# Optimization experiments

Measured on AMD Instinct MI355X. Metric: run time of the kernel, lower is better.

The kernel has to match this reference:

```python
import jax, jax.numpy as jnp
import numpy as np

B, S, D = 2, 2048, 1024
H, KD, VD = 16, 64, 64


def setup_inputs() -> dict:
    key = jax.random.key(0)
    ks = jax.random.split(key, 12)
    s = 1.0 / np.sqrt(D)
    return {
        "q": jax.random.normal(ks[0], (B, S, D), jnp.float32),
        "k": jax.random.normal(ks[1], (B, S, D), jnp.float32),
        "v": jax.random.normal(ks[2], (B, S, D), jnp.float32),
        "mask": jnp.ones((S, S), jnp.int32),
        "Wq": jax.random.normal(ks[3], (D, H * KD), jnp.float32) * s,
        "bq": jnp.zeros((H * KD,), jnp.float32),
        "Wk": jax.random.normal(ks[4], (D, H * KD), jnp.float32) * s,
        "bk": jnp.zeros((H * KD,), jnp.float32),
        "Wv": jax.random.normal(ks[5], (D, H * VD), jnp.float32) * s,
        "bv": jnp.zeros((H * VD,), jnp.float32),
        "Wo": jax.random.normal(ks[6], (H * VD, D), jnp.float32) * (1.0 / np.sqrt(H * VD)),
        "bo": jnp.zeros((D,), jnp.float32),
    }


def reference(q, k, v, mask, Wq, bq, Wk, bk, Wv, bv, Wo, bo):
    bs = q.shape[0]
    # projections -> [B, H, S, d]
    qh = (q @ Wq + bq).reshape(bs, -1, H, KD).transpose(0, 2, 1, 3)
    kh = (k @ Wk + bk).reshape(bs, -1, H, KD).transpose(0, 2, 1, 3)
    vh = (v @ Wv + bv).reshape(bs, -1, H, VD).transpose(0, 2, 1, 3)
    scores = jnp.einsum("bhqd,bhkd->bhqk", qh, kh) / np.sqrt(KD)
    scores = jnp.where(mask[None, None, :, :] == 0, -1e9, scores)
    probs = jax.nn.softmax(scores, axis=-1)  # dropout is identity in eval
    attn = jnp.einsum("bhqk,bhkd->bhqd", probs, vh)
    concat = attn.transpose(0, 2, 1, 3).reshape(bs, -1, H * VD)
    return concat @ Wo + bo
```

## Files before the change

### kernel.cpp

```cpp
#include <hip/hip_runtime.h>
#include <stdint.h>

typedef __attribute__((ext_vector_type(8))) short short8;
typedef __attribute__((ext_vector_type(4))) float f32x4;
typedef __attribute__((ext_vector_type(16))) float f32x16;
typedef __attribute__((ext_vector_type(2))) unsigned int u32x2;

constexpr int Bc = 2, Sc = 2048, Dc = 1024, Hc = 16;
constexpr int MR = Bc * Sc;
#define CSC 0.18033688011112042f

static __device__ __forceinline__ unsigned short f2bf(float f) {
    union { float f; uint32_t u; } v; v.f = f;
    uint32_t u = v.u;
    u += 0x7FFFu + ((u >> 16) & 1u);
    return (unsigned short)(u >> 16);
}

static __device__ __forceinline__ uint32_t cvtpk(float lo, float hi) {
    uint32_t r;
    asm("v_cvt_pk_bf16_f32 %0, %1, %2" : "=v"(r) : "v"(lo), "v"(hi));
    return r;
}

static __device__ __forceinline__ float exp2a(float x) {
    float r;
    asm("v_exp_f32 %0, %1" : "=v"(r) : "v"(x));
    return r;
}

static __device__ __forceinline__ void gload_lds16(const void* g, void* l) {
    __builtin_amdgcn_global_load_lds(
        (const __attribute__((address_space(1))) unsigned int*)g,
        (__attribute__((address_space(3))) unsigned int*)l, 16, 0, 0);
}

__global__ void transpose_w_kernel(const float* __restrict__ Wq, const float* __restrict__ Wk,
                                   const float* __restrict__ Wv, const float* __restrict__ Wo,
                                   unsigned short* __restrict__ out) {
    __shared__ unsigned short tile[64][65];
    const float* W = (blockIdx.z == 0) ? Wq : (blockIdx.z == 1) ? Wk
                   : (blockIdx.z == 2) ? Wv : Wo;
    unsigned short* Wt = out + (size_t)blockIdx.z * (size_t)Dc * Dc;
    int n0 = blockIdx.x * 64, k0 = blockIdx.y * 64;
    int c = threadIdx.x & 63, r0 = threadIdx.x >> 6;
#pragma unroll
    for (int rr = 0; rr < 16; rr++) {
        int r = r0 + rr * 4;
        tile[r][c] = f2bf(W[(size_t)(k0 + r) * Dc + n0 + c]);
    }
    __syncthreads();
#pragma unroll
    for (int rr = 0; rr < 16; rr++) {
        int r = r0 + rr * 4;
        Wt[(size_t)(n0 + r) * Dc + k0 + c] = tile[c][r];
    }
}

__global__ __launch_bounds__(256, 2)
void gemm_qkv_kernel(const float* __restrict__ Xq, const float* __restrict__ Xk,
                     const float* __restrict__ Xv,
                     const unsigned short* __restrict__ Wt,
                     const float* __restrict__ bq, const float* __restrict__ bk,
                     const float* __restrict__ bv,
                     unsigned short* __restrict__ Qp,
                     unsigned short* __restrict__ Kp,
                     unsigned short* __restrict__ Vt)
{
    __shared__ unsigned short POOL[24576];
    unsigned short* Alds = POOL;
    unsigned short* Bl0  = POOL + 8192;
    unsigned short* Bl1  = POOL + 16384;
    const int lane = threadIdx.x & 63;
    const int wave = threadIdx.x >> 6;
    const int g = lane >> 4, r = lane & 15;
    const int r7 = r & 7;
    const int wr = wave >> 1, wc = wave & 1;
    const int tM = blockIdx.x * 128, tN = blockIdx.y * 128;
    const int m_blk = tN >> 10;
    const float* Af = (m_blk == 0) ? Xq : (m_blk == 1) ? Xk : Xv;
    const float* bias = (m_blk == 0) ? bq : (m_blk == 1) ? bk : bv;

    f32x4 acc[4][4] = {};

    const int lrow = lane >> 3, lun = lane & 7;
    const int lswz = (lun ^ lrow) * 8;
    const float* asrc[4];
    const unsigned short* bsrc[4];
#pragma unroll
    for (int i = 0; i < 4; i++) {
        int c = wave * 4 + i;
        int row = c * 8 + lrow;
        asrc[i] = Af + (size_t)(tM + row) * 1024 + lun * 8;
        bsrc[i] = Wt + (size_t)(tN + row) * 1024 + lswz;
    }

#pragma unroll
    for (int i = 0; i < 4; i++)
        gload_lds16(bsrc[i], (void*)(Bl0 + (wave * 4 + i) * 512));
    __builtin_amdgcn_sched_barrier(0);
    float4 afA[4][2];
#pragma unroll
    for (int i = 0; i < 4; i++) {
        afA[i][0] = *(const float4*)(asrc[i]);
        afA[i][1] = *(const float4*)(asrc[i] + 4);
    }

    unsigned short* Bcur = Bl0;
    unsigned short* Bnxt = Bl1;

    int sw[2];
    sw[0] = ((0 * 4 + g) ^ r7) * 8;
    sw[1] = ((1 * 4 + g) ^ r7) * 8;

    for (int kt = 0; kt < 1024; kt += 64) {
        if (kt < 960) {
#pragma unroll
            for (int i = 0; i < 4; i++)
                gload_lds16(bsrc[i] + kt + 64, (void*)(Bnxt + (wave * 4 + i) * 512));
        }
        __builtin_amdgcn_sched_barrier(0);

#pragma unroll
        for (int i = 0; i < 4; i++) {
            int c = wave * 4 + i;
            union { uint32_t u[4]; short8 s; } pk;
            pk.u[0] = cvtpk(afA[i][0].x, afA[i][0].y);
            pk.u[1] = cvtpk(afA[i][0].z, afA[i][0].w);
            pk.u[2] = cvtpk(afA[i][1].x, afA[i][1].y);
            pk.u[3] = cvtpk(afA[i][1].z, afA[i][1].w);
            *(short8*)(Alds + c * 512 + lrow * 64 + lswz) = pk.s;
        }
        if (kt < 960) {
#pragma unroll
            for (int i = 0; i < 4; i++) {
                afA[i][0] = *(const float4*)(asrc[i] + kt + 64);
                afA[i][1] = *(const float4*)(asrc[i] + kt + 68);
            }
        }
        __builtin_amdgcn_sched_barrier(0);
        asm volatile("s_waitcnt lgkmcnt(0)" ::: "memory");
        __builtin_amdgcn_s_barrier();
        __builtin_amdgcn_sched_barrier(0);

#pragma unroll
        for (int ks = 0; ks < 2; ks++) {
            short8 av[4], bvv[4];
#pragma unroll
            for (int mf = 0; mf < 4; mf++)
                av[mf] = *(const short8*)(Alds + (wr * 64 + mf * 16 + r) * 64 + sw[ks]);
#pragma unroll
            for (int nf = 0; nf < 4; nf++)
                bvv[nf] = *(const short8*)(Bcur + (wc * 64 + nf * 16 + r) * 64 + sw[ks]);
#pragma unroll
            for (int mf = 0; mf < 4; mf++)
#pragma unroll
                for (int nf = 0; nf < 4; nf++)
                    acc[mf][nf] = __builtin_amdgcn_mfma_f32_16x16x32_bf16(av[mf], bvv[nf], acc[mf][nf], 0, 0, 0);
        }
        __builtin_amdgcn_sched_barrier(0);
        asm volatile("s_waitcnt lgkmcnt(0)" ::: "memory");
        __builtin_amdgcn_s_barrier();
        __builtin_amdgcn_sched_barrier(0);

        unsigned short* tb = Bcur; Bcur = Bnxt; Bnxt = tb;
    }

    const int cbase = (tN & 1023) + wc * 64;
    const int h = cbase >> 6;
    const int bblk = tM >> 11;
    const int tMs = tM & 2047;
    unsigned short* Ow = POOL + wave * 2304;
    const float scl = (m_blk == 0) ? CSC : 1.0f;

    if (m_blk < 2) {
        unsigned short* dstQ = (m_blk == 0) ? Qp : Kp;
#pragma unroll
        for (int p = 0; p < 2; p++) {
#pragma unroll
            for (int mf2 = 0; mf2 < 2; mf2++)
#pragma unroll
                for (int nf = 0; nf < 4; nf++)
#pragma unroll
                    for (int i = 0; i < 4; i++) {
                        float val = (acc[2 * p + mf2][nf][i] + bias[cbase + nf * 16 + r]) * scl;
                        Ow[(mf2 * 16 + g * 4 + i) * 72 + nf * 16 + r] = f2bf(val);
                    }
            asm volatile("s_waitcnt lgkmcnt(0)" ::: "memory");
#pragma unroll
            for (int r4 = 0; r4 < 4; r4++) {
                int sl = r4 * 8 + (lane >> 3), dc = (lane & 7) * 8;
                short8 vv = *(const short8*)(Ow + sl * 72 + dc);
                int s = tMs + wr * 64 + p * 32 + sl;
                *(short8*)(dstQ + (((size_t)(bblk * Hc + h)) * Sc + s) * 64 + dc) = vv;
            }
            asm volatile("s_waitcnt lgkmcnt(0)" ::: "memory");
        }
    } else {
#pragma unroll
        for (int p = 0; p < 2; p++) {
#pragma unroll
            for (int nf2 = 0; nf2 < 2; nf2++)
#pragma unroll
                for (int mf = 0; mf < 4; mf++)
#pragma unroll
                    for (int i = 0; i < 4; i++) {
                        float val = acc[mf][2 * p + nf2][i] + bias[cbase + (2 * p + nf2) * 16 + r];
                        Ow[(nf2 * 16 + r) * 72 + mf * 16 + g * 4 + i] = f2bf(val);
                    }
            asm volatile("s_waitcnt lgkmcnt(0)" ::: "memory");
#pragma unroll
            for (int r4 = 0; r4 < 4; r4++) {
                int dl = r4 * 8 + (lane >> 3), sc_ = (lane & 7) * 8;
                short8 vv = *(const short8*)(Ow + dl * 72 + sc_);
                int dk = p * 32 + dl;
                *(short8*)(Vt + ((size_t)(bblk * Hc + h) * 64 + dk) * Sc
                              + (tMs + wr * 64 + sc_)) = vv;
            }
            asm volatile("s_waitcnt lgkmcnt(0)" ::: "memory");
        }
    }
}

__global__ __launch_bounds__(256, 2)
void gemm_out_kernel(const unsigned short* __restrict__ A,
                     const unsigned short* __restrict__ Bt,
                     const float* __restrict__ bias,
                     float* __restrict__ Cout)
{
    __shared__ unsigned short Alds[128 * 64];
    __shared__ unsigned short Blds[128 * 64];
    const int lane = threadIdx.x & 63;
    const int wave = threadIdx.x >> 6;
    const int g = lane >> 4, r = lane & 15;
    const int wr = wave >> 1, wc = wave & 1;
    const int tM = blockIdx.x * 128, tN = blockIdx.y * 128;

    f32x4 acc[4][4] = {};

    for (int kt = 0; kt < 1024; kt += 64) {
        __syncthreads();
#pragma unroll
        for (int i = 0; i < 4; i++) {
            int c = wave * 4 + i;
            int row = c * 8 + (lane >> 3);
            int kcol = kt + (lane & 7) * 8;
            gload_lds16(A  + (size_t)(tM + row) * 1024 + kcol, (void*)(Alds + c * 512));
            gload_lds16(Bt + (size_t)(tN + row) * 1024 + kcol, (void*)(Blds + c * 512));
        }
        __syncthreads();
#pragma unroll
        for (int ks = 0; ks < 2; ks++) {
            short8 av[4], bvv[4];
#pragma unroll
            for (int mf = 0; mf < 4; mf++)
                av[mf] = *(const short8*)(Alds + (wr * 64 + mf * 16 + r) * 64 + ks * 32 + g * 8);
#pragma unroll
            for (int nf = 0; nf < 4; nf++)
                bvv[nf] = *(const short8*)(Blds + (wc * 64 + nf * 16 + r) * 64 + ks * 32 + g * 8);
#pragma unroll
            for (int mf = 0; mf < 4; mf++)
#pragma unroll
                for (int nf = 0; nf < 4; nf++)
                    acc[mf][nf] = __builtin_amdgcn_mfma_f32_16x16x32_bf16(av[mf], bvv[nf], acc[mf][nf], 0, 0, 0);
        }
    }

#pragma unroll
    for (int mf = 0; mf < 4; mf++)
#pragma unroll
      for (int nf = 0; nf < 4; nf++)
#pragma unroll
        for (int i = 0; i < 4; i++) {
            int row = tM + wr * 64 + mf * 16 + g * 4 + i;
            int col = tN + wc * 64 + nf * 16 + r;
            Cout[(size_t)row * 1024 + col] = acc[mf][nf][i] + bias[col];
        }
}

__global__ __launch_bounds__(512, 4)
void attn_kernel(const unsigned short* __restrict__ Qp,
                 const unsigned short* __restrict__ Kp,
                 const unsigned short* __restrict__ Vt,
                 unsigned short* __restrict__ Oc)
{
    __shared__ __align__(16) unsigned short SH[2][3][64 * 72];

    const int tid = threadIdx.x;
    const int wave = tid >> 6, lane = tid & 63;
    const int ql = lane & 31, h5 = lane >> 5;
    const int half = wave >> 2;
    const int bh = blockIdx.y;
    const int qbw = blockIdx.x * 128 + (wave & 3) * 32;

    const unsigned short* Kg = Kp + (size_t)bh * Sc * 64 + (size_t)half * 1024 * 64;
    const unsigned short* Vg = Vt + (size_t)bh * (size_t)64 * Sc + half * 1024;

    const unsigned short* Qrow = Qp + ((size_t)bh * Sc + qbw + ql) * 64 + h5 * 8;
    short8 qf[4];
#pragma unroll
    for (int ks = 0; ks < 4; ks++) qf[ks] = *(const short8*)(Qrow + ks * 16);

    unsigned short* Kc = &SH[half][0][0];
    unsigned short* Kn = &SH[half][1][0];
    unsigned short* Vl = &SH[half][2][0];
    const int fro = ql * 72 + h5 * 8;

    const int t8 = tid & 255;
    const int srow = t8 >> 3, sc8 = (t8 & 7) * 8;
    const int stl = srow * 72 + sc8;
    const unsigned short* kgp = Kg + srow * 64 + sc8;
    const unsigned short* vg0 = Vg + (size_t)srow * Sc + sc8;
    const unsigned short* vg1 = Vg + (size_t)(32 + srow) * Sc + sc8;

    f32x16 ot0{}, ot1{};
    f32x16 st0{}, st1{};
    float lsum = 0.f;

    short8 ka = *(const short8*)(kgp);
    short8 kb2 = *(const short8*)(kgp + 2048);
    *(short8*)(Kc + stl) = ka;  *(short8*)(Kc + stl + 2304) = kb2;
    asm volatile("s_waitcnt lgkmcnt(0)" ::: "memory");
    __builtin_amdgcn_s_barrier();
    ka  = *(const short8*)(kgp + 4096);
    kb2 = *(const short8*)(kgp + 4096 + 2048);
    short8 va  = *(const short8*)(vg0);
    short8 vb2 = *(const short8*)(vg1);
    __builtin_amdgcn_s_setprio(1);
#pragma unroll
    for (int ks = 0; ks < 4; ks++) {
        short8 a0 = *(const short8*)(Kc + fro + ks * 16);
        st0 = __builtin_amdgcn_mfma_f32_32x32x16_bf16(a0, qf[ks], st0, 0, 0, 0);
        short8 a1 = *(const short8*)(Kc + fro + 2304 + ks * 16);
        st1 = __builtin_amdgcn_mfma_f32_32x32x16_bf16(a1, qf[ks], st1, 0, 0, 0);
    }
    __builtin_amdgcn_s_setprio(0);

    for (int t = 0; t < 16; ++t) {
        if (t < 15) { *(short8*)(Kn + stl) = ka;  *(short8*)(Kn + stl + 2304) = kb2; }
        *(short8*)(Vl + stl) = va;  *(short8*)(Vl + stl + 2304) = vb2;
        asm volatile("s_waitcnt lgkmcnt(0)" ::: "memory");
        __builtin_amdgcn_s_barrier();

        if (t < 14) {
            ka  = *(const short8*)(kgp + (t + 2) * 4096);
            kb2 = *(const short8*)(kgp + (t + 2) * 4096 + 2048);
        }
        if (t < 15) {
            va  = *(const short8*)(vg0 + (t + 1) * 64);
            vb2 = *(const short8*)(vg1 + (t + 1) * 64);
        }

        float ps = 0.f;
#pragma unroll
        for (int c4 = 0; c4 < 4; c4++) {
            const f32x16& sv = (c4 < 2) ? st0 : st1;
            const int s8 = (c4 & 1) * 8;
            float e0 = exp2a(sv[s8 + 0]), e1 = exp2a(sv[s8 + 1]);
            float e2 = exp2a(sv[s8 + 2]), e3 = exp2a(sv[s8 + 3]);
            float e4 = exp2a(sv[s8 + 4]), e5 = exp2a(sv[s8 + 5]);
            float e6 = exp2a(sv[s8 + 6]), e7 = exp2a(sv[s8 + 7]);
            ps += ((e0 + e1) + (e2 + e3)) + ((e4 + e5) + (e6 + e7));
            uint32_t c0 = cvtpk(e0, e1), c1 = cvtpk(e2, e3);
            uint32_t c2 = cvtpk(e4, e5), c3 = cvtpk(e6, e7);
            asm("v_permlane32_swap_b32 %0, %1" : "+v"(c0), "+v"(c2));
            asm("v_permlane32_swap_b32 %0, %1" : "+v"(c1), "+v"(c3));
            union { uint32_t u[4]; short8 s; } bf;
            bf.u[0] = c0; bf.u[1] = c1; bf.u[2] = c2; bf.u[3] = c3;
            __builtin_amdgcn_s_setprio(1);
            short8 a0 = *(const short8*)(Vl + fro + c4 * 16);
            ot0 = __builtin_amdgcn_mfma_f32_32x32x16_bf16(a0, bf.s, ot0, 0, 0, 0);
            short8 a1 = *(const short8*)(Vl + fro + 2304 + c4 * 16);
            ot1 = __builtin_amdgcn_mfma_f32_32x32x16_bf16(a1, bf.s, ot1, 0, 0, 0);
            __builtin_amdgcn_s_setprio(0);
        }
        ps += __shfl_xor(ps, 32);
        lsum += ps;

        if (t < 15) {
            st0 = f32x16{}; st1 = f32x16{};
            __builtin_amdgcn_s_setprio(1);
#pragma unroll
            for (int ks = 0; ks < 4; ks++) {
                short8 a0 = *(const short8*)(Kn + fro + ks * 16);
                st0 = __builtin_amdgcn_mfma_f32_32x32x16_bf16(a0, qf[ks], st0, 0, 0, 0);
                short8 a1 = *(const short8*)(Kn + fro + 2304 + ks * 16);
                st1 = __builtin_amdgcn_mfma_f32_32x32x16_bf16(a1, qf[ks], st1, 0, 0, 0);
            }
            __builtin_amdgcn_s_setprio(0);
        }

        __builtin_amdgcn_s_barrier();
        unsigned short* tswp = Kc; Kc = Kn; Kn = tswp;
    }

    float* Olds = (float*)&SH[0][0][0];
    float* Lld  = (float*)((char*)&SH[0][0][0] + 33792);
    __syncthreads();
    if (h5 == 0) Lld[wave * 32 + ql] = lsum;
    __syncthreads();
    float l2 = Lld[(wave ^ 4) * 32 + ql];
    if (wave >= 4) {
        float* dst = Olds + (size_t)(wave - 4) * (64 * 33) + ql;
#pragma unroll
        for (int i = 0; i < 16; i++) {
            int d0 = (i & 3) + 8 * (i >> 2) + 4 * h5;
            dst[d0 * 33]        = ot0[i];
            dst[(d0 + 32) * 33] = ot1[i];
        }
    }
    __syncthreads();
    if (wave < 4) {
        float inv = 1.0f / (lsum + l2);
        const float* src = Olds + (size_t)wave * (64 * 33) + ql;
#pragma unroll
        for (int i = 0; i < 16; i++) {
            int d0 = (i & 3) + 8 * (i >> 2) + 4 * h5;
            ot0[i] = (ot0[i] + src[d0 * 33]) * inv;
            ot1[i] = (ot1[i] + src[(d0 + 32) * 33]) * inv;
        }
        asm volatile("s_waitcnt lgkmcnt(0)" ::: "memory");
        __builtin_amdgcn_sched_barrier(0);
        unsigned short* Ost = (unsigned short*)(Olds + (size_t)wave * (64 * 33));
#pragma unroll
        for (int dt = 0; dt < 2; dt++)
#pragma unroll
            for (int t = 0; t < 4; t++) {
                const f32x16& o = dt ? ot1 : ot0;
                uint32_t w0 = cvtpk(o[4 * t + 0], o[4 * t + 1]);
                uint32_t w1 = cvtpk(o[4 * t + 2], o[4 * t + 3]);
                *(u32x2*)(Ost + ql * 72 + dt * 32 + t * 8 + h5 * 4) = u32x2{w0, w1};
            }
        asm volatile("s_waitcnt lgkmcnt(0)" ::: "memory");
        __builtin_amdgcn_sched_barrier(0);
        int r = lane >> 1, cb = (lane & 1) * 4;
        int b = bh >> 4, hh = bh & 15;
        unsigned short* dstg = Oc + ((size_t)b * Sc + qbw + r) * (Hc * 64) + hh * 64;
#pragma unroll
        for (int t = 0; t < 4; t++)
            *(short8*)(dstg + (cb + t) * 8) = *(const short8*)(Ost + r * 72 + (cb + t) * 8);
    }
}

extern "C" void kernel_launch(void* const* d_in, const int* in_sizes, int n_in,
                              void* d_out, int out_size, void* d_ws, size_t ws_size,
                              hipStream_t stream)
{
    (void)in_sizes; (void)n_in; (void)out_size; (void)ws_size;
    const float* q  = (const float*)d_in[0];
    const float* k  = (const float*)d_in[1];
    const float* v  = (const float*)d_in[2];
    const float* Wq = (const float*)d_in[4];
    const float* bq = (const float*)d_in[5];
    const float* Wk = (const float*)d_in[6];
    const float* bk = (const float*)d_in[7];
    const float* Wv = (const float*)d_in[8];
    const float* bv = (const float*)d_in[9];
    const float* Wo = (const float*)d_in[10];
    const float* bo = (const float*)d_in[11];

    char* ws = (char*)d_ws;
    unsigned short* Wt    = (unsigned short*)(ws);
    unsigned short* Qp    = (unsigned short*)(ws + (size_t)8  * 1024 * 1024);
    unsigned short* Kp    = (unsigned short*)(ws + (size_t)16 * 1024 * 1024);
    unsigned short* Vtg   = (unsigned short*)(ws + (size_t)24 * 1024 * 1024);
    unsigned short* attnC = (unsigned short*)(ws + (size_t)32 * 1024 * 1024);

    transpose_w_kernel<<<dim3(16, 16, 4), 256, 0, stream>>>(Wq, Wk, Wv, Wo, Wt);

    gemm_qkv_kernel<<<dim3(32, 24), 256, 0, stream>>>(q, k, v, Wt, bq, bk, bv, Qp, Kp, Vtg);

    attn_kernel<<<dim3(16, 32), 512, 0, stream>>>(Qp, Kp, Vtg, attnC);

    gemm_out_kernel<<<dim3(32, 8), 256, 0, stream>>>(attnC, Wt + 3 * 1048576, bo, (float*)d_out);
}
```

Baseline: 113.8 us.

## Double-buffer LDS tiles with swizzled layout in output projection GEMM

The output GEMM now prefetches the next K-tile into a second LDS buffer while computing the current one, using vmcnt waits and raw barriers instead of two syncthreads per step. The LDS layout is XOR-swizzled on 16-byte chunks so that MFMA operand reads avoid bank conflicts. This doubles LDS usage per block, which may reduce occupancy, and the manual waitcnt scheduling adds fragility.

```diff
diff --git a/kernel.cpp b/kernel.cpp
--- a/kernel.cpp
+++ b/kernel.cpp
@@ -228,42 +228,77 @@
                      const float* __restrict__ bias,
                      float* __restrict__ Cout)
 {
-    __shared__ unsigned short Alds[128 * 64];
-    __shared__ unsigned short Blds[128 * 64];
+    __shared__ unsigned short Al[2][8192];
+    __shared__ unsigned short Bl[2][8192];
     const int lane = threadIdx.x & 63;
     const int wave = threadIdx.x >> 6;
     const int g = lane >> 4, r = lane & 15;
+    const int r7 = r & 7;
     const int wr = wave >> 1, wc = wave & 1;
     const int tM = blockIdx.x * 128, tN = blockIdx.y * 128;
 
     f32x4 acc[4][4] = {};
 
+    const int lrow = lane >> 3, lun = lane & 7;
+    const int lswz = (lun ^ lrow) * 8;
+    const unsigned short* asrc[4];
+    const unsigned short* bsrc[4];
+#pragma unroll
+    for (int i = 0; i < 4; i++) {
+        int c = wave * 4 + i;
+        int row = c * 8 + lrow;
+        asrc[i] = A  + (size_t)(tM + row) * 1024 + lswz;
+        bsrc[i] = Bt + (size_t)(tN + row) * 1024 + lswz;
+    }
+
+#pragma unroll
+    for (int i = 0; i < 4; i++) {
+        gload_lds16(asrc[i], (void*)(Al[0] + (wave * 4 + i) * 512));
+        gload_lds16(bsrc[i], (void*)(Bl[0] + (wave * 4 + i) * 512));
+    }
+    __builtin_amdgcn_sched_barrier(0);
+
+    int sw[2];
+    sw[0] = ((0 * 4 + g) ^ r7) * 8;
+    sw[1] = ((1 * 4 + g) ^ r7) * 8;
+
     for (int kt = 0; kt < 1024; kt += 64) {
-        __syncthreads();
-#pragma unroll
-        for (int i = 0; i < 4; i++) {
-            int c = wave * 4 + i;
-            int row = c * 8 + (lane >> 3);
-            int kcol = kt + (lane & 7) * 8;
-            gload_lds16(A  + (size_t)(tM + row) * 1024 + kcol, (void*)(Alds + c * 512));
-            gload_lds16(Bt + (size_t)(tN + row) * 1024 + kcol, (void*)(Blds + c * 512));
-        }
-        __syncthreads();
+        const int cur = (kt >> 6) & 1;
+        if (kt < 960) {
+#pragma unroll
+            for (int i = 0; i < 4; i++) {
+                gload_lds16(asrc[i] + kt + 64, (void*)(Al[cur ^ 1] + (wave * 4 + i) * 512));
+                gload_lds16(bsrc[i] + kt + 64, (void*)(Bl[cur ^ 1] + (wave * 4 + i) * 512));
+            }
+        }
+        __builtin_amdgcn_sched_barrier(0);
+        if (kt < 960) {
+            asm volatile("s_waitcnt vmcnt(8)" ::: "memory");
+        } else {
+            asm volatile("s_waitcnt vmcnt(0)" ::: "memory");
+        }
+        __builtin_amdgcn_s_barrier();
+        __builtin_amdgcn_sched_barrier(0);
+
 #pragma unroll
         for (int ks = 0; ks < 2; ks++) {
             short8 av[4], bvv[4];
 #pragma unroll
             for (int mf = 0; mf < 4; mf++)
-                av[mf] = *(const short8*)(Alds + (wr * 64 + mf * 16 + r) * 64 + ks * 32 + g * 8);
+                av[mf] = *(const short8*)(Al[cur] + (wr * 64 + mf * 16 + r) * 64 + sw[ks]);
 #pragma unroll
             for (int nf = 0; nf < 4; nf++)
-                bvv[nf] = *(const short8*)(Blds + (wc * 64 + nf * 16 + r) * 64 + ks * 32 + g * 8);
+                bvv[nf] = *(const short8*)(Bl[cur] + (wc * 64 + nf * 16 + r) * 64 + sw[ks]);
 #pragma unroll
             for (int mf = 0; mf < 4; mf++)
 #pragma unroll
                 for (int nf = 0; nf < 4; nf++)
                     acc[mf][nf] = __builtin_amdgcn_mfma_f32_16x16x32_bf16(av[mf], bvv[nf], acc[mf][nf], 0, 0, 0);
         }
+        __builtin_amdgcn_sched_barrier(0);
+        asm volatile("s_waitcnt lgkmcnt(0)" ::: "memory");
+        __builtin_amdgcn_s_barrier();
+        __builtin_amdgcn_sched_barrier(0);
     }
 
 #pragma unroll
```

Result: faster. 110.3 us (-3.1%).
